# Kernel optimization log

Hardware: AMD Instinct MI355X
Metric: run time of the kernel (lower is better)

The kernel has to match this reference:

```python
import jax, jax.numpy as jnp
import numpy as np

B = 256        # batch_size
T = 256        # max_length
H = 1024       # hidden width (hardcoded in module)
NOISE = 128    # noise_depth
NOUT = 100     # n_outputs
EPS = 1e-5     # BatchNorm1d default eps
SLOPE = 0.01   # LeakyReLU default negative_slope


def _bn(x, g, b):
    # BatchNorm1d in training mode: biased batch stats over dim 0
    m = jnp.mean(x, axis=0)
    v = jnp.var(x, axis=0)
    return (x - m) * jax.lax.rsqrt(v + EPS) * g + b


def setup_inputs() -> dict:
    key = jax.random.key(0)
    ks = jax.random.split(key, 16)
    s = 0.02
    d = {
        "z": jax.random.normal(ks[0], (B, NOISE), jnp.float32),
        # projection linears (torch Linear weight layout: [out, in])
        "W_zh": jax.random.normal(ks[1], (H, NOISE), jnp.float32) * s,
        "b_zh": jnp.zeros((H,), jnp.float32),
        "W_zc": jax.random.normal(ks[2], (H, NOISE), jnp.float32) * s,
        "b_zc": jnp.zeros((H,), jnp.float32),
        # BN affine params (torch default init: gamma=1, beta=0)
        "g_bnzh": jnp.ones((H,), jnp.float32), "b_bnzh": jnp.zeros((H,), jnp.float32),
        "g_bnzc": jnp.ones((H,), jnp.float32), "b_bnzc": jnp.zeros((H,), jnp.float32),
        # LSTMCell params, gate order i,f,g,o
        "W_ih": jax.random.normal(ks[3], (4 * H, H), jnp.float32) * s,
        "b_ih": jnp.zeros((4 * H,), jnp.float32),
        "W_hh": jax.random.normal(ks[4], (4 * H, H), jnp.float32) * s,
        "b_hh": jnp.zeros((4 * H,), jnp.float32),
        "g_bn0": jnp.ones((H,), jnp.float32), "b_bn0": jnp.zeros((H,), jnp.float32),
        "W1": jax.random.normal(ks[5], (512, H), jnp.float32) * s,
        "b1": jnp.zeros((512,), jnp.float32),
        "g_bn1": jnp.ones((512,), jnp.float32), "b_bn1": jnp.zeros((512,), jnp.float32),
        "W2": jax.random.normal(ks[6], (256, 512), jnp.float32) * s,
        "b2": jnp.zeros((256,), jnp.float32),
        "g_bn2": jnp.ones((256,), jnp.float32), "b_bn2": jnp.zeros((256,), jnp.float32),
        "W3": jax.random.normal(ks[7], (NOUT, 256), jnp.float32) * s,
        "b3": jnp.zeros((NOUT,), jnp.float32),
        # 'go' token: one-hot [1,0,...,0] tiled over batch
        "go": jnp.zeros((B, H), jnp.float32).at[:, 0].set(1.0),
    }
    return d


def reference(z, W_zh, b_zh, W_zc, b_zc, g_bnzh, b_bnzh, g_bnzc, b_bnzc,
              W_ih, b_ih, W_hh, b_hh, g_bn0, b_bn0, W1, b1, g_bn1, b_bn1,
              W2, b2, g_bn2, b_bn2, W3, b3, go):
    zh = _bn(z @ W_zh.T + b_zh, g_bnzh, b_bnzh)   # initial h
    zc = _bn(z @ W_zc.T + b_zc, g_bnzc, b_bnzc)   # initial c

    def step(carry, _):
        h, c, x = carry
        gates = x @ W_ih.T + b_ih + h @ W_hh.T + b_hh  # [B, 4H]
        i, f, g, o = jnp.split(gates, 4, axis=1)
        c2 = jax.nn.sigmoid(f) * c + jax.nn.sigmoid(i) * jnp.tanh(g)
        h2 = jax.nn.sigmoid(o) * jnp.tanh(c2)
        return (h2, c2, h2), h2  # next input is h2 (out = hx)

    _, ys = jax.lax.scan(step, (zh, zc, go), None, length=T)  # ys: [T, B, H]

    # torch: output = stack(dim=2) -> [B, H, T]; then view(-1, H) on raw memory
    output = jnp.transpose(ys, (1, 2, 0))          # [B, H, T] contiguous
    output_stack = output.reshape(-1, H)           # faithful raw reshape (mixes H and T)

    o1 = jax.nn.leaky_relu(_bn(output_stack, g_bn0, b_bn0) @ W1.T + b1, SLOPE)
    o2 = jax.nn.leaky_relu(_bn(o1, g_bn1, b_bn1) @ W2.T + b2, SLOPE)
    o3 = _bn(o2, g_bn2, b_bn2) @ W3.T + b3          # [B*T*?, NOUT] flat

    output_unstack = o3.reshape(B, -1, T)           # [B, NOUT, T]
    return jax.nn.softmax(output_unstack, axis=1)
```

## Files before the change

### kernel.cpp

```cpp
#include <hip/hip_runtime.h>
#include <hip/hip_bf16.h>

typedef __attribute__((ext_vector_type(8))) short bf16x8;
typedef __attribute__((ext_vector_type(4))) float f32x4;

#define NBLK 256

__device__ inline unsigned short f2b(float x){
  union { float f; unsigned int u; } v; v.f = x;
  unsigned int u = v.u;
  return (unsigned short)((u + 0x7FFFu + ((u >> 16) & 1u)) >> 16);
}
__device__ inline float b2f(unsigned short h){
  union { unsigned int u; float f; } v; v.u = ((unsigned int)h) << 16; return v.f;
}
__device__ inline float sigm(float x){ return 1.f / (1.f + __expf(-x)); }
__device__ inline float tanh_f(float x){ float e2 = __expf(2.f * x); return 1.f - 2.f / (e2 + 1.f); }

__global__ __launch_bounds__(256) void zerofill(float* __restrict__ p, int n){
  int i = blockIdx.x * 256 + threadIdx.x;
  if (i < n) p[i] = 0.f;
}

__device__ inline int packrow(int n){
  int g = n >> 10, h = n & 1023;
  return (h >> 3) * 32 + (h & 7) * 4 + g;
}

__global__ __launch_bounds__(256) void prep_w(
    const float* __restrict__ Wih, const float* __restrict__ Whh,
    const float* __restrict__ bih, const float* __restrict__ bhh,
    unsigned short* __restrict__ Wsum_p, unsigned short* __restrict__ Whh_b,
    float* __restrict__ bias_sp)
{
  size_t idx = (size_t)blockIdx.x * 256 + threadIdx.x;
  int n = (int)(idx >> 10), k = (int)(idx & 1023);
  int g = n >> 10, h = n & 1023;
  float wi = Wih[idx], wh = Whh[idx];
  int htile = h >> 3;
  int r  = ((h & 7) << 2) | g;
  int nt = r >> 4, lr2 = r & 15;
  int kb = k >> 5, lg2 = (k >> 3) & 3, e = k & 7;
  size_t dest = (size_t)htile * 32768 + (size_t)nt * 16384 + (size_t)kb * 512
              + (size_t)(lg2 * 16 + lr2) * 8 + e;
  Wsum_p[dest] = f2b(wi + wh);
  Whh_b[idx] = f2b(wh);
  if (idx < 4096) bias_sp[packrow((int)idx)] = bih[idx] + bhh[idx];
}

__global__ __launch_bounds__(256) void prep_b0(
    const float* __restrict__ Wih, const float* __restrict__ go,
    const float* __restrict__ bih, const float* __restrict__ bhh,
    float* __restrict__ bias0)
{
  __shared__ float red[4];
  int n = blockIdx.x, t = threadIdx.x;
  float acc = 0.f;
  for (int k = t; k < 1024; k += 256) acc += Wih[(size_t)n*1024 + k] * go[k];
  for (int off = 32; off > 0; off >>= 1) acc += __shfl_down(acc, off, 64);
  if ((t & 63) == 0) red[t >> 6] = acc;
  __syncthreads();
  if (t == 0) bias0[n] = bih[n] + bhh[n] + red[0] + red[1] + red[2] + red[3];
}

__global__ __launch_bounds__(256) void zproj(
    const float* __restrict__ z, const float* __restrict__ Wzh, const float* __restrict__ bzh,
    const float* __restrict__ Wzc, const float* __restrict__ bzc,
    float* __restrict__ zh_raw, float* __restrict__ zc_raw)
{
  int idx = blockIdx.x * 256 + threadIdx.x;
  int b = idx >> 10, c = idx & 1023;
  const float* zr = z + b * 128;
  const float* wh = Wzh + c * 128;
  const float* wc = Wzc + c * 128;
  float s1 = bzh[c], s2 = bzc[c];
  #pragma unroll 8
  for (int k = 0; k < 128; k++){ float zv = zr[k]; s1 += zv * wh[k]; s2 += zv * wc[k]; }
  zh_raw[idx] = s1; zc_raw[idx] = s2;
}

__global__ __launch_bounds__(256) void bn_init(
    const float* __restrict__ zh_raw, const float* __restrict__ zc_raw,
    const float* __restrict__ g_h, const float* __restrict__ bt_h,
    const float* __restrict__ g_c, const float* __restrict__ bt_c,
    unsigned short* __restrict__ zh_b, float* __restrict__ c_f)
{
  __shared__ float red[4][4];
  int c = blockIdx.x, r = threadIdx.x;
  float v1 = zh_raw[r * 1024 + c];
  float v2 = zc_raw[r * 1024 + c];
  float s[4] = { v1, v1*v1, v2, v2*v2 };
  #pragma unroll
  for (int i = 0; i < 4; i++){
    float x = s[i];
    for (int off = 32; off > 0; off >>= 1) x += __shfl_down(x, off, 64);
    if ((r & 63) == 0) red[i][r >> 6] = x;
  }
  __syncthreads();
  float m1 = (red[0][0]+red[0][1]+red[0][2]+red[0][3]) * (1.f/256.f);
  float q1 = (red[1][0]+red[1][1]+red[1][2]+red[1][3]) * (1.f/256.f);
  float m2 = (red[2][0]+red[2][1]+red[2][2]+red[2][3]) * (1.f/256.f);
  float q2 = (red[3][0]+red[3][1]+red[3][2]+red[3][3]) * (1.f/256.f);
  float var1 = q1 - m1*m1; if (var1 < 0.f) var1 = 0.f;
  float var2 = q2 - m2*m2; if (var2 < 0.f) var2 = 0.f;
  float a1 = g_h[c] * rsqrtf(var1 + 1e-5f), be1 = bt_h[c] - m1*a1;
  float a2 = g_c[c] * rsqrtf(var2 + 1e-5f), be2 = bt_c[c] - m2*a2;
  zh_b[r * 1024 + c] = f2b(v1*a1 + be1);
  c_f[r * 1024 + c] = v2*a2 + be2;
}

template<int K, int ACT, int OBF16>
__global__ __launch_bounds__(256) void gemm_bt2(
    const unsigned short* __restrict__ A, const unsigned short* __restrict__ B,
    const float* __restrict__ bias, void* __restrict__ outp, int N)
{
  const int tid = threadIdx.x;
  const int w = tid >> 6, l = tid & 63;
  const int lr = l & 15, lg = l >> 4;
  const int m0 = blockIdx.y * 64 + (w >> 1) * 32;
  const int n0 = blockIdx.x * 128 + (w & 1) * 64;
  f32x4 acc[2][4];
  #pragma unroll
  for (int i = 0; i < 2; i++)
    #pragma unroll
    for (int j = 0; j < 4; j++) acc[i][j] = (f32x4){0.f,0.f,0.f,0.f};

  const unsigned short* pa0 = A + (size_t)(m0 + lr) * K + lg * 8;
  const unsigned short* pa1 = pa0 + (size_t)16 * K;
  const unsigned short* pb0 = B + (size_t)(n0 + lr) * K + lg * 8;

  for (int kb = 0; kb < K; kb += 32){
    bf16x8 a0 = *(const bf16x8*)(pa0 + kb);
    bf16x8 a1 = *(const bf16x8*)(pa1 + kb);
    bf16x8 b0 = *(const bf16x8*)(pb0 + kb);
    bf16x8 b1 = *(const bf16x8*)(pb0 + (size_t)16 * K + kb);
    bf16x8 b2 = *(const bf16x8*)(pb0 + (size_t)32 * K + kb);
    bf16x8 b3 = *(const bf16x8*)(pb0 + (size_t)48 * K + kb);
    acc[0][0] = __builtin_amdgcn_mfma_f32_16x16x32_bf16(a0, b0, acc[0][0], 0, 0, 0);
    acc[0][1] = __builtin_amdgcn_mfma_f32_16x16x32_bf16(a0, b1, acc[0][1], 0, 0, 0);
    acc[0][2] = __builtin_amdgcn_mfma_f32_16x16x32_bf16(a0, b2, acc[0][2], 0, 0, 0);
    acc[0][3] = __builtin_amdgcn_mfma_f32_16x16x32_bf16(a0, b3, acc[0][3], 0, 0, 0);
    acc[1][0] = __builtin_amdgcn_mfma_f32_16x16x32_bf16(a1, b0, acc[1][0], 0, 0, 0);
    acc[1][1] = __builtin_amdgcn_mfma_f32_16x16x32_bf16(a1, b1, acc[1][1], 0, 0, 0);
    acc[1][2] = __builtin_amdgcn_mfma_f32_16x16x32_bf16(a1, b2, acc[1][2], 0, 0, 0);
    acc[1][3] = __builtin_amdgcn_mfma_f32_16x16x32_bf16(a1, b3, acc[1][3], 0, 0, 0);
  }

  #pragma unroll
  for (int mi = 0; mi < 2; mi++)
    #pragma unroll
    for (int ni = 0; ni < 4; ni++){
      int col = n0 + ni * 16 + lr;
      float bs = bias[col];
      #pragma unroll
      for (int j = 0; j < 4; j++){
        int row = m0 + mi * 16 + lg * 4 + j;
        float v = acc[mi][ni][j] + bs;
        if (ACT) v = v > 0.f ? v : 0.01f * v;
        if (OBF16) ((unsigned short*)outp)[(size_t)row * N + col] = f2b(v);
        else       ((float*)outp)[(size_t)row * N + col] = v;
      }
    }
}

__global__ __launch_bounds__(256) void lstm_cell0(
    const float* __restrict__ gates, float* __restrict__ c,
    unsigned short* __restrict__ hbuf0)
{
  int idx = blockIdx.x * 256 + threadIdx.x;
  int b = idx >> 10, h = idx & 1023;
  const float* g = gates + (size_t)b * 4096;
  float ig = g[h], fg = g[1024 + h], gg = g[2048 + h], og = g[3072 + h];
  float co = c[idx];
  float c2 = sigm(fg) * co + sigm(ig) * tanh_f(gg);
  float h2 = sigm(og) * tanh_f(c2);
  c[idx] = c2;
  hbuf0[idx] = f2b(h2);
}

__global__ __launch_bounds__(512, 1) void lstm_persist(
    const unsigned short* __restrict__ Wp, const float* __restrict__ bias_sp,
    unsigned short* __restrict__ hbuf0, unsigned short* __restrict__ hbuf1,
    const float* __restrict__ c_init, unsigned short* __restrict__ ys,
    unsigned int* __restrict__ arr)
{
  __shared__ unsigned short Wl[32768];
  __shared__ unsigned short chunk[1024][20];
  const int tid = threadIdx.x;
  const int blk = blockIdx.x;
  const int mhalf = blk >> 7;
  const int htile = blk & 127;
  const int w = tid >> 6, l = tid & 63;
  const int lr = l & 15, lg = l >> 4;
  const int m0 = mhalf * 128;

  {
    const bf16x8* src = (const bf16x8*)(Wp + (size_t)htile * 32768);
    bf16x8* dst = (bf16x8*)Wl;
    for (int i = tid; i < 4096; i += 512) dst[i] = src[i];
  }
  for (int i = tid; i < 1024; i += 512){
    int b = i >> 3, hl = i & 7;
    chunk[i][0] = hbuf0[(size_t)(m0 + b) * 1024 + htile * 8 + hl];
  }

  const int hw0 = lr >> 2;
  float bb[2];
  bb[0] = bias_sp[htile * 32 + lr];
  bb[1] = bias_sp[htile * 32 + 16 + lr];

  float creg[2][4];
  #pragma unroll
  for (int ni = 0; ni < 2; ni++)
    #pragma unroll
    for (int j = 0; j < 4; j++){
      int row = m0 + w * 16 + lg * 4 + j;
      int h = htile * 8 + ni * 4 + hw0;
      creg[ni][j] = c_init[(size_t)row * 1024 + h];
    }

  __syncthreads();

  const char* lwb = (const char*)Wl + l * 16;

  #pragma unroll 1
  for (int t = 1; t < 256; t++){
    const unsigned short* hin = (t & 1) ? hbuf0 : hbuf1;
    unsigned int* hout32 = (unsigned int*)((t & 1) ? hbuf1 : hbuf0);

    f32x4 acc[2];
    acc[0] = (f32x4){0.f,0.f,0.f,0.f};
    acc[1] = (f32x4){0.f,0.f,0.f,0.f};

    const unsigned short* pa0 = hin + (size_t)(m0 + w * 16 + lr) * 1024 + lg * 8;

    #pragma unroll 8
    for (int kb = 0; kb < 32; kb++){
      bf16x8 a0 = *(const bf16x8*)(pa0 + kb * 32);
      bf16x8 b0 = *(const bf16x8*)(lwb + kb * 1024);
      bf16x8 b1 = *(const bf16x8*)(lwb + 32768 + kb * 1024);
      acc[0] = __builtin_amdgcn_mfma_f32_16x16x32_bf16(a0, b0, acc[0], 0, 0, 0);
      acc[1] = __builtin_amdgcn_mfma_f32_16x16x32_bf16(a0, b1, acc[1], 0, 0, 0);
    }

    #pragma unroll
    for (int ni = 0; ni < 2; ni++)
      #pragma unroll
      for (int j = 0; j < 4; j++){
        float v = acc[ni][j] + bb[ni];
        float va = v;
        float vb = __shfl_xor(v, 1);
        float vc = __shfl_xor(v, 2);
        float vd = __shfl_xor(vb, 2);
        bool s1 = (lr & 1), s2 = (lr & 2);
        float P1 = s2 ? vc : va, P2 = s2 ? vd : vb;
        float Q1 = s2 ? va : vc, Q2 = s2 ? vb : vd;
        float gi  = s1 ? P2 : P1;
        float gf  = s1 ? P1 : P2;
        float gg  = s1 ? Q2 : Q1;
        float go_ = s1 ? Q1 : Q2;
        float c2 = sigm(gf) * creg[ni][j] + sigm(gi) * tanh_f(gg);
        float h2 = sigm(go_) * tanh_f(c2);
        creg[ni][j] = c2;
        unsigned short hb = f2b(h2);
        int rl = w * 16 + lg * 4 + j;
        int hl = ni * 4 + hw0;
        if ((lr & 3) == 0) chunk[rl * 8 + hl][t & 15] = hb;
        unsigned int pv = (unsigned int)(unsigned short)__shfl_xor((int)hb, 4);
        if ((lr & 7) == 1){
          unsigned int val = (pv << 16) | (unsigned int)hb;
          atomicExch(&hout32[(m0 + rl) * 512 + htile * 4 + ni * 2 + (hw0 >> 1)], val);
        }
      }

    __syncthreads();
    if (t < 255 && tid == 0)
      __hip_atomic_fetch_add(&arr[blk * 32], 1u, __ATOMIC_RELAXED, __HIP_MEMORY_SCOPE_AGENT);

    if ((t & 15) == 15){
      int t0 = t - 15;
      for (int r = tid; r < 1024; r += 512){
        int b = r >> 3, hl = r & 7;
        uint2 p0 = *(const uint2*)&chunk[r][0];
        uint2 p1 = *(const uint2*)&chunk[r][4];
        uint2 p2 = *(const uint2*)&chunk[r][8];
        uint2 p3 = *(const uint2*)&chunk[r][12];
        size_t o = ((size_t)(m0 + b) * 1024 + htile * 8 + hl) * 256 + t0;
        *(uint4*)&ys[o]     = (uint4){p0.x, p0.y, p1.x, p1.y};
        *(uint4*)&ys[o + 8] = (uint4){p2.x, p2.y, p3.x, p3.y};
      }
    }

    if (t < 255){
      if (tid < NBLK){
        int spin = 0;
        while (__hip_atomic_fetch_add(&arr[tid * 32], 0u, __ATOMIC_RELAXED,
                                      __HIP_MEMORY_SCOPE_AGENT) < (unsigned)t
               && spin < (1 << 16)) ++spin;
      }
      __syncthreads();
      if (tid == 0) __builtin_amdgcn_fence(__ATOMIC_ACQUIRE, "agent");
      __syncthreads();
    }
  }
}

template<int C>
__global__ __launch_bounds__(256) void stats1(
    const unsigned short* __restrict__ X, float* __restrict__ psum, float* __restrict__ psq)
{
  int col = blockIdx.x * 256 + threadIdx.x;
  int r0 = blockIdx.y * 256;
  float s = 0.f, q = 0.f;
  for (int r = r0; r < r0 + 256; r++){
    float v = b2f(X[(size_t)r * C + col]);
    s += v; q += v * v;
  }
  psum[(size_t)blockIdx.y * C + col] = s;
  psq [(size_t)blockIdx.y * C + col] = q;
}

__global__ __launch_bounds__(256) void stats2(
    const float* __restrict__ psum, const float* __restrict__ psq,
    const float* __restrict__ g, const float* __restrict__ b,
    float* __restrict__ alpha, float* __restrict__ beta, int C)
{
  int c = blockIdx.x * 256 + threadIdx.x;
  if (c >= C) return;
  float s = 0.f, q = 0.f;
  for (int i = 0; i < 256; i++){ s += psum[(size_t)i * C + c]; q += psq[(size_t)i * C + c]; }
  float m = s * (1.f / 65536.f);
  float var = q * (1.f / 65536.f) - m * m; if (var < 0.f) var = 0.f;
  float a = g[c] * rsqrtf(var + 1e-5f);
  alpha[c] = a; beta[c] = b[c] - m * a;
}

template<int K>
__global__ __launch_bounds__(256) void foldk(
    const float* __restrict__ W, const float* __restrict__ bias,
    const float* __restrict__ alpha, const float* __restrict__ beta,
    unsigned short* __restrict__ Wb, float* __restrict__ bp, int rows)
{
  __shared__ float red[4];
  int o = blockIdx.x, t = threadIdx.x;
  float acc = 0.f;
  if (o < rows){
    for (int j = t; j < K; j += 256){
      float wv = W[(size_t)o * K + j];
      acc += beta[j] * wv;
      Wb[(size_t)o * K + j] = f2b(wv * alpha[j]);
    }
  } else {
    for (int j = t; j < K; j += 256) Wb[(size_t)o * K + j] = 0;
  }
  for (int off = 32; off > 0; off >>= 1) acc += __shfl_down(acc, off, 64);
  if ((t & 63) == 0) red[t >> 6] = acc;
  __syncthreads();
  if (t == 0) bp[o] = (o < rows ? bias[o] : 0.f) + red[0] + red[1] + red[2] + red[3];
}

__global__ __launch_bounds__(256) void softmax_k(
    const unsigned short* __restrict__ o3p, float* __restrict__ out)
{
  __shared__ unsigned short tile[25600];
  int b = blockIdx.x, t = threadIdx.x;
  const unsigned short* src = o3p + (size_t)b * 256 * 128;
  for (int i = t; i < 25600; i += 256){
    int rr = i / 100, nc = i - rr * 100;
    tile[i] = src[rr * 128 + nc];
  }
  __syncthreads();
  int v = t;
  float mx = -1e30f;
  for (int u = 0; u < 100; u++) mx = fmaxf(mx, b2f(tile[u * 256 + v]));
  float s = 0.f;
  for (int u = 0; u < 100; u++) s += __expf(b2f(tile[u * 256 + v]) - mx);
  float inv = 1.f / s;
  float* dst = out + (size_t)b * 25600;
  for (int u = 0; u < 100; u++)
    dst[u * 256 + v] = __expf(b2f(tile[u * 256 + v]) - mx) * inv;
}

extern "C" void kernel_launch(void* const* d_in, const int* in_sizes, int n_in,
                              void* d_out, int out_size, void* d_ws, size_t ws_size,
                              hipStream_t stream)
{
  (void)in_sizes; (void)n_in;
  const float* z     = (const float*)d_in[0];
  const float* Wzh   = (const float*)d_in[1];
  const float* bzh   = (const float*)d_in[2];
  const float* Wzc   = (const float*)d_in[3];
  const float* bzc   = (const float*)d_in[4];
  const float* g_bnzh= (const float*)d_in[5];
  const float* b_bnzh= (const float*)d_in[6];
  const float* g_bnzc= (const float*)d_in[7];
  const float* b_bnzc= (const float*)d_in[8];
  const float* Wih   = (const float*)d_in[9];
  const float* bih   = (const float*)d_in[10];
  const float* Whh   = (const float*)d_in[11];
  const float* bhh   = (const float*)d_in[12];
  const float* g_bn0 = (const float*)d_in[13];
  const float* b_bn0 = (const float*)d_in[14];
  const float* W1    = (const float*)d_in[15];
  const float* b1    = (const float*)d_in[16];
  const float* g_bn1 = (const float*)d_in[17];
  const float* b_bn1 = (const float*)d_in[18];
  const float* W2    = (const float*)d_in[19];
  const float* b2    = (const float*)d_in[20];
  const float* g_bn2 = (const float*)d_in[21];
  const float* b_bn2 = (const float*)d_in[22];
  const float* W3    = (const float*)d_in[23];
  const float* b3    = (const float*)d_in[24];
  const float* go    = (const float*)d_in[25];

  char* base = (char*)d_ws;
  size_t off = 0;
  auto alloc = [&](size_t bytes)->char*{
    char* p = base + off;
    off = (off + bytes + 255) & ~(size_t)255;
    return p;
  };
  const size_t MB = 1024 * 1024;

  unsigned short* ys = (unsigned short*)alloc(128 * MB);
  unsigned short* o1 = (unsigned short*)alloc(64 * MB);
  char* zone = alloc(32 * MB);
  unsigned short* Wsum_p = (unsigned short*)(zone);
  unsigned short* Whh_b  = (unsigned short*)(zone + 8 * MB);
  float*          gates0 = (float*)(zone + 16 * MB);
  float* zh_raw = (float*)alloc(1 * MB);
  float* zc_raw = (float*)alloc(1 * MB);
  float* bias_sp = (float*)alloc(16384);
  float* bias0   = (float*)alloc(16384);
  unsigned short* zh_b  = (unsigned short*)alloc((size_t)256 * 1024 * 2);
  unsigned short* hbuf0 = (unsigned short*)alloc((size_t)256 * 1024 * 2);
  unsigned short* hbuf1 = (unsigned short*)alloc((size_t)256 * 1024 * 2);
  float* c_f    = (float*)alloc((size_t)256 * 1024 * 4);
  float* psum   = (float*)alloc(1 * MB);
  float* psq    = (float*)alloc(1 * MB);
  float* alpha0 = (float*)alloc(4096); float* beta0 = (float*)alloc(4096);
  float* alpha1 = (float*)alloc(4096); float* beta1 = (float*)alloc(4096);
  float* alpha2 = (float*)alloc(4096); float* beta2 = (float*)alloc(4096);
  unsigned short* W1b = (unsigned short*)alloc((size_t)512 * 1024 * 2);
  unsigned short* W2b = (unsigned short*)alloc((size_t)256 * 512 * 2);
  unsigned short* W3b = (unsigned short*)alloc((size_t)128 * 256 * 2);
  float* b1p = (float*)alloc(4096);
  float* b2p = (float*)alloc(4096);
  float* b3p = (float*)alloc(4096);
  unsigned int* arr = (unsigned int*)alloc(32768);
  unsigned short* o2  = (unsigned short*)zone;
  unsigned short* o3p = o1;

  if (off > ws_size){
    zerofill<<<(out_size + 255) / 256, 256, 0, stream>>>((float*)d_out, out_size);
    return;
  }

  zerofill<<<32, 256, 0, stream>>>((float*)arr, 8192);
  prep_w<<<16384, 256, 0, stream>>>(Wih, Whh, bih, bhh, Wsum_p, Whh_b, bias_sp);
  prep_b0<<<4096, 256, 0, stream>>>(Wih, go, bih, bhh, bias0);
  zproj<<<1024, 256, 0, stream>>>(z, Wzh, bzh, Wzc, bzc, zh_raw, zc_raw);
  bn_init<<<1024, 256, 0, stream>>>(zh_raw, zc_raw, g_bnzh, b_bnzh, g_bnzc, b_bnzc, zh_b, c_f);

  gemm_bt2<1024, 0, 0><<<dim3(32, 4), 256, 0, stream>>>(zh_b, Whh_b, bias0, gates0, 4096);
  lstm_cell0<<<1024, 256, 0, stream>>>(gates0, c_f, hbuf0);

  lstm_persist<<<NBLK, 512, 0, stream>>>(Wsum_p, bias_sp, hbuf0, hbuf1, c_f, ys, arr);

  stats1<1024><<<dim3(4, 256), 256, 0, stream>>>(ys, psum, psq);
  stats2<<<4, 256, 0, stream>>>(psum, psq, g_bn0, b_bn0, alpha0, beta0, 1024);
  foldk<1024><<<512, 256, 0, stream>>>(W1, b1, alpha0, beta0, W1b, b1p, 512);
  gemm_bt2<1024, 1, 1><<<dim3(4, 1024), 256, 0, stream>>>(ys, W1b, b1p, o1, 512);

  stats1<512><<<dim3(2, 256), 256, 0, stream>>>(o1, psum, psq);
  stats2<<<2, 256, 0, stream>>>(psum, psq, g_bn1, b_bn1, alpha1, beta1, 512);
  foldk<512><<<256, 256, 0, stream>>>(W2, b2, alpha1, beta1, W2b, b2p, 256);
  gemm_bt2<512, 1, 1><<<dim3(2, 1024), 256, 0, stream>>>(o1, W2b, b2p, o2, 256);

  stats1<256><<<dim3(1, 256), 256, 0, stream>>>(o2, psum, psq);
  stats2<<<1, 256, 0, stream>>>(psum, psq, g_bn2, b_bn2, alpha2, beta2, 256);
  foldk<256><<<128, 256, 0, stream>>>(W3, b3, alpha2, beta2, W3b, b3p, 100);
  gemm_bt2<256, 0, 1><<<dim3(1, 1024), 256, 0, stream>>>(o2, W3b, b3p, o3p, 128);

  softmax_k<<<256, 256, 0, stream>>>(o3p, (float*)d_out);
}
```

Measured before the change: 4.166 ms.

## Replace all-to-all spin barrier with per-half leader gather/release barrier

Before, every block of the persistent LSTM kernel polled all 256 arrival counters at every timestep. Now the barrier is split by batch half, since the two halves are independent. In each half, two leader blocks poll the 128 arrival counters, then bump per-block release counters that the other blocks poll with a single thread using s_sleep backoff. This is meant to cut heavy atomic polling traffic and contention on the counters, at the cost of an extra signalling hop of latency on each step.

```diff
diff --git a/kernel.cpp b/kernel.cpp
--- a/kernel.cpp
+++ b/kernel.cpp
@@ -182,7 +182,7 @@
     const unsigned short* __restrict__ Wp, const float* __restrict__ bias_sp,
     unsigned short* __restrict__ hbuf0, unsigned short* __restrict__ hbuf1,
     const float* __restrict__ c_init, unsigned short* __restrict__ ys,
-    unsigned int* __restrict__ arr)
+    unsigned int* __restrict__ arr, unsigned int* __restrict__ rel)
 {
   __shared__ unsigned short Wl[32768];
   __shared__ unsigned short chunk[1024][20];
@@ -193,6 +193,9 @@
   const int w = tid >> 6, l = tid & 63;
   const int lr = l & 15, lg = l >> 4;
   const int m0 = mhalf * 128;
+  const int halfbase = mhalf << 7;
+  const int lid = blk - halfbase;
+  const bool leader = (lid < 2);
 
   {
     const bf16x8* src = (const bf16x8*)(Wp + (size_t)htile * 32768);
@@ -292,13 +295,33 @@
     }
 
     if (t < 255){
-      if (tid < NBLK){
-        int spin = 0;
-        while (__hip_atomic_fetch_add(&arr[tid * 32], 0u, __ATOMIC_RELAXED,
-                                      __HIP_MEMORY_SCOPE_AGENT) < (unsigned)t
-               && spin < (1 << 16)) ++spin;
+      if (leader){
+        if (tid < 128){
+          int spin = 0;
+          while (__hip_atomic_fetch_add(&arr[(halfbase + tid) * 32], 0u,
+                                        __ATOMIC_RELAXED, __HIP_MEMORY_SCOPE_AGENT)
+                     < (unsigned)t
+                 && spin < (1 << 16)){
+            __builtin_amdgcn_s_sleep(1);
+            ++spin;
+          }
+        }
+        __syncthreads();
+        if (tid < 64)
+          __hip_atomic_fetch_add(&rel[(halfbase + lid * 64 + tid) * 32], 1u,
+                                 __ATOMIC_RELAXED, __HIP_MEMORY_SCOPE_AGENT);
+      } else {
+        if (tid == 0){
+          int spin = 0;
+          while (__hip_atomic_fetch_add(&rel[blk * 32], 0u,
+                                        __ATOMIC_RELAXED, __HIP_MEMORY_SCOPE_AGENT)
+                     < (unsigned)t
+                 && spin < (1 << 16)){
+            __builtin_amdgcn_s_sleep(1);
+            ++spin;
+          }
+        }
       }
-      __syncthreads();
       if (tid == 0) __builtin_amdgcn_fence(__ATOMIC_ACQUIRE, "agent");
       __syncthreads();
     }
@@ -448,6 +471,7 @@
   float* b2p = (float*)alloc(4096);
   float* b3p = (float*)alloc(4096);
   unsigned int* arr = (unsigned int*)alloc(32768);
+  unsigned int* rel = (unsigned int*)alloc(32768);
   unsigned short* o2  = (unsigned short*)zone;
   unsigned short* o3p = o1;
 
@@ -456,7 +480,7 @@
     return;
   }
 
-  zerofill<<<32, 256, 0, stream>>>((float*)arr, 8192);
+  zerofill<<<64, 256, 0, stream>>>((float*)arr, 16384);
   prep_w<<<16384, 256, 0, stream>>>(Wih, Whh, bih, bhh, Wsum_p, Whh_b, bias_sp);
   prep_b0<<<4096, 256, 0, stream>>>(Wih, go, bih, bhh, bias0);
   zproj<<<1024, 256, 0, stream>>>(z, Wzh, bzh, Wzc, bzc, zh_raw, zc_raw);
@@ -465,7 +489,7 @@
   gemm_bt2<1024, 0, 0><<<dim3(32, 4), 256, 0, stream>>>(zh_b, Whh_b, bias0, gates0, 4096);
   lstm_cell0<<<1024, 256, 0, stream>>>(gates0, c_f, hbuf0);
 
-  lstm_persist<<<NBLK, 512, 0, stream>>>(Wsum_p, bias_sp, hbuf0, hbuf1, c_f, ys, arr);
+  lstm_persist<<<NBLK, 512, 0, stream>>>(Wsum_p, bias_sp, hbuf0, hbuf1, c_f, ys, arr, rel);
 
   stats1<1024><<<dim3(4, 256), 256, 0, stream>>>(ys, psum, psq);
   stats2<<<4, 256, 0, stream>>>(psum, psq, g_bn0, b_bn0, alpha0, beta0, 1024);
```

After: 3.985 ms (median of 2 runs). 1.05x faster.
